# Optimization experiments

Hardware: AMD Instinct MI355X
Metric: run time of the kernel (lower is better)

## Reference

```python
import jax, jax.numpy as jnp
import numpy as np

WIDTH = 64  # attention_width

def setup_inputs() -> dict:
    key = jax.random.key(0)
    ks = jax.random.split(key, 4)
    B, T, D, U = 4, 1024, 1024, 64
    x = jax.random.normal(ks[0], (B, T, D), dtype=jnp.float32)
    Wt = jax.random.normal(ks[1], (D, U), dtype=jnp.float32) * (1.0 / np.sqrt(D))
    Wx = jax.random.normal(ks[2], (D, U), dtype=jnp.float32) * (1.0 / np.sqrt(D))
    bh = jnp.zeros((U,), dtype=jnp.float32)
    Wa = jax.random.normal(ks[3], (U, 1), dtype=jnp.float32) * (1.0 / np.sqrt(U))
    ba = jnp.zeros((1,), dtype=jnp.float32)
    return {"x": x, "Wt": Wt, "Wx": Wx, "bh": bh, "Wa": Wa, "ba": ba}


def reference(x, Wt, Wx, bh, Wa, ba):
    B, T, D = x.shape
    # additive emission: h = tanh(q_i + k_j + bh), e_ij = h @ Wa + ba
    q = jnp.einsum('btd,du->btu', x, Wt)  # [B,T,U]
    k = jnp.einsum('btd,du->btu', x, Wx)  # [B,T,U]
    h = jnp.tanh(q[:, :, None, :] + k[:, None, :, :] + bh)  # [B,T,T,U]
    e = jnp.einsum('btsu,uo->bts', h, Wa) + ba[0]  # [B,T,T]
    # local-width band mask (width centered, history_only=False)
    idx = jnp.arange(T)
    lower = (idx - WIDTH // 2)[:, None]           # [T,1]
    upper = lower + WIDTH
    band = (lower <= idx[None, :]) & (idx[None, :] < upper)  # [T,T]
    e = e - 10000.0 * (1.0 - band.astype(e.dtype))
    a = jax.nn.softmax(e, axis=-1)  # [B,T,T]
    v = jnp.einsum('bts,bsd->btd', a, x)
    return v
```

## Files before the change

### kernel.cpp

```cpp
#include <hip/hip_runtime.h>

#define BB 4
#define TT 1024
#define DD 1024
#define UU 64
#define HW 32

typedef unsigned short u16;
typedef __attribute__((ext_vector_type(4))) unsigned short u16x4;
typedef __attribute__((ext_vector_type(8))) unsigned short u16x8;
typedef __attribute__((ext_vector_type(8))) short bf16x8;
typedef __attribute__((ext_vector_type(4))) float f32x4;

__device__ __forceinline__ u16 bf16_rne(float f) {
  unsigned b = __builtin_bit_cast(unsigned, f);
  b += 0x7FFFu + ((b >> 16) & 1u);
  return (u16)(b >> 16);
}
__device__ __forceinline__ float bf16_tof(u16 h) {
  return __builtin_bit_cast(float, ((unsigned)h) << 16);
}

#define WLD 65
__global__ __launch_bounds__(256) void wprep_kernel(
    const float* __restrict__ Wt, const float* __restrict__ Wx,
    u16* __restrict__ Wht, u16* __restrict__ Wlt)
{
  __shared__ float ws[128 * WLD];
  const int tid = threadIdx.x;
  const int d0  = blockIdx.x * 128;
  const float* __restrict__ src = blockIdx.y ? Wx : Wt;

  for (int i = tid; i < 2048; i += 256) {
    int r  = i >> 4;
    int c4 = (i & 15) << 2;
    float4 v = *(const float4*)(src + (size_t)(d0 + r) * UU + c4);
    float* w = ws + r * WLD + c4;
    w[0] = v.x; w[1] = v.y; w[2] = v.z; w[3] = v.w;
  }
  __syncthreads();

  for (int it = tid; it < 1024; it += 256) {
    int u = it >> 4, oct = it & 15;
    u16x8 h, l;
    #pragma unroll
    for (int j = 0; j < 8; ++j) {
      float v = ws[(8 * oct + j) * WLD + u];
      u16 hh = bf16_rne(v);
      h[j] = hh;
      l[j] = bf16_rne(v - bf16_tof(hh));
    }
    size_t off = (size_t)(blockIdx.y * UU + u) * DD + d0 + 8 * oct;
    *(u16x8*)(Wht + off) = h;
    *(u16x8*)(Wlt + off) = l;
  }
}

#define PROWS 16
#define XLD (DD + 8)

__global__ __launch_bounds__(512) void proj_mfma_kernel(
    const float* __restrict__ x, const u16* __restrict__ Wht,
    const u16* __restrict__ Wlt, float* __restrict__ qo, float* __restrict__ ko)
{
  __shared__ __align__(16) u16 Xh[PROWS][XLD];
  __shared__ __align__(16) u16 Xl[PROWS][XLD];

  const int tid  = threadIdx.x;
  const int row0 = blockIdx.x * PROWS;

  {
    const float4* src = (const float4*)(x + (size_t)row0 * DD);
    #pragma unroll
    for (int i = 0; i < 8; ++i) {
      int idx4 = tid + 512 * i;
      int r    = idx4 >> 8;
      int k4   = (idx4 & 255) << 2;
      float4 v = src[idx4];
      float vv[4] = {v.x, v.y, v.z, v.w};
      u16x4 hv, lv;
      #pragma unroll
      for (int j = 0; j < 4; ++j) {
        u16 hh = bf16_rne(vv[j]);
        float lf = vv[j] - bf16_tof(hh);
        hv[j] = hh;
        lv[j] = bf16_rne(lf);
      }
      *(u16x4*)&Xh[r][k4] = hv;
      *(u16x4*)&Xl[r][k4] = lv;
    }
  }
  __syncthreads();

  const int lane = tid & 63;
  const int wv   = tid >> 6;
  const int arow = lane & 15;
  const int g    = lane >> 4;
  const int u0   = wv * 16;

  const u16* ah_p = &Xh[arow][8 * g];
  const u16* al_p = &Xl[arow][8 * g];
  const u16* bh_p = Wht + (size_t)(u0 + arow) * DD + 8 * g;
  const u16* bl_p = Wlt + (size_t)(u0 + arow) * DD + 8 * g;

  f32x4 acc0 = {0.f, 0.f, 0.f, 0.f};
  f32x4 acc1 = {0.f, 0.f, 0.f, 0.f};
  f32x4 acc2 = {0.f, 0.f, 0.f, 0.f};
  f32x4 acc3 = {0.f, 0.f, 0.f, 0.f};

  #pragma unroll 8
  for (int ks = 0; ks < 32; ++ks) {
    bf16x8 ah = *(const bf16x8*)(ah_p + 32 * ks);
    bf16x8 al = *(const bf16x8*)(al_p + 32 * ks);
    bf16x8 bh = *(const bf16x8*)(bh_p + 32 * ks);
    bf16x8 bl = *(const bf16x8*)(bl_p + 32 * ks);
    acc0 = __builtin_amdgcn_mfma_f32_16x16x32_bf16(ah, bh, acc0, 0, 0, 0);
    acc1 = __builtin_amdgcn_mfma_f32_16x16x32_bf16(ah, bl, acc1, 0, 0, 0);
    acc2 = __builtin_amdgcn_mfma_f32_16x16x32_bf16(al, bh, acc2, 0, 0, 0);
    acc3 = __builtin_amdgcn_mfma_f32_16x16x32_bf16(al, bl, acc3, 0, 0, 0);
  }

  const int col = u0 + arow;
  float* dst = (col < UU) ? (qo + col) : (ko + (col - UU));
  #pragma unroll
  for (int r = 0; r < 4; ++r) {
    dst[(size_t)(row0 + 4 * g + r) * UU] = acc0[r] + acc1[r] + acc2[r] + acc3[r];
  }
}

__global__ __launch_bounds__(512) void band_kernel(
    const float* __restrict__ x,  const float* __restrict__ qi,
    const float* __restrict__ ki, const float* __restrict__ bh,
    const float* __restrict__ Wa, const float* __restrict__ ba,
    float* __restrict__ out)
{
  __shared__ __align__(16) float eq[8 * UU];
  __shared__ __align__(16) float ek[72 * UU];
  __shared__ __align__(16) float at[72 * 8];

  const int tid  = threadIdx.x;
  const int bid  = blockIdx.x;
  const int tile = (bid & 7) * 64 + (bid >> 3);
  const int b    = tile >> 7;
  const int i0   = (tile & 127) * 8;

  const int jlo = max(0, i0 - HW);
  const int jhi = min(TT, i0 + 8 - 1 + HW);
  const int NJ  = jhi - jlo;

  {
    if (tid < 128) {
      float4 qv = ((const float4*)(qi + (size_t)(b * TT + i0) * UU))[tid];
      float4 bv = ((const float4*)bh)[tid & 15];
      float4 ev;
      ev.x = __expf(-2.0f * (qv.x + bv.x));
      ev.y = __expf(-2.0f * (qv.y + bv.y));
      ev.z = __expf(-2.0f * (qv.z + bv.z));
      ev.w = __expf(-2.0f * (qv.w + bv.w));
      ((float4*)eq)[tid] = ev;
    }
    const float4* ksrc = (const float4*)(ki + (size_t)(b * TT + jlo) * UU);
    const int nk4 = NJ * (UU / 4);
    for (int i2 = tid; i2 < nk4; i2 += 512) {
      float4 kv = ksrc[i2];
      float4 ev;
      ev.x = __expf(-2.0f * kv.x);
      ev.y = __expf(-2.0f * kv.y);
      ev.z = __expf(-2.0f * kv.z);
      ev.w = __expf(-2.0f * kv.w);
      ((float4*)ek)[i2] = ev;
    }
  }
  __syncthreads();

  const float bav = ba[0];

  {
    const int w    = tid >> 6;
    const int lane = tid & 63;
    const int g    = lane >> 3;
    const int uc   = (lane & 7) * 8;
    float eqv[8], wv[8];
    {
      float4 a0 = *(const float4*)(eq + g * UU + uc);
      float4 a1 = *(const float4*)(eq + g * UU + uc + 4);
      eqv[0] = a0.x; eqv[1] = a0.y; eqv[2] = a0.z; eqv[3] = a0.w;
      eqv[4] = a1.x; eqv[5] = a1.y; eqv[6] = a1.z; eqv[7] = a1.w;
      float4 wa0 = *(const float4*)(Wa + uc);
      float4 wa1 = *(const float4*)(Wa + uc + 4);
      wv[0] = wa0.x; wv[1] = wa0.y; wv[2] = wa0.z; wv[3] = wa0.w;
      wv[4] = wa1.x; wv[5] = wa1.y; wv[6] = wa1.z; wv[7] = wa1.w;
    }
    const int ig = i0 + g;
    for (int j = w; j < NJ; j += 8) {
      const float* kp = ek + j * UU + uc;
      float4 k0 = *(const float4*)kp;
      float4 k1 = *(const float4*)(kp + 4);
      float ekv[8] = {k0.x, k0.y, k0.z, k0.w, k1.x, k1.y, k1.z, k1.w};
      float s0 = 0.f;
      #pragma unroll
      for (int s = 0; s < 8; ++s) {
        float t  = eqv[s] * ekv[s];
        float th = (1.0f - t) * __builtin_amdgcn_rcpf(1.0f + t);
        s0 = __builtin_fmaf(th, wv[s], s0);
      }
      s0 += __shfl_xor(s0, 1);
      s0 += __shfl_xor(s0, 2);
      s0 += __shfl_xor(s0, 4);
      const int jg = jlo + j;
      const bool inband = (jg >= ig - HW) && (jg < ig + HW);
      if ((lane & 7) == 0) at[j * 8 + g] = inband ? (s0 + bav) : -1e30f;
    }
  }
  __syncthreads();

  {
    const int row = tid >> 6;
    const int l   = tid & 63;
    float v0 = (l      < NJ) ? at[(l     ) * 8 + row] : -1e30f;
    float v1 = (l + 64 < NJ) ? at[(l + 64) * 8 + row] : -1e30f;
    float m = fmaxf(v0, v1);
    #pragma unroll
    for (int off = 32; off >= 1; off >>= 1) m = fmaxf(m, __shfl_xor(m, off));
    float e0 = __expf(v0 - m);
    float e1 = __expf(v1 - m);
    float ssum = e0 + e1;
    #pragma unroll
    for (int off = 32; off >= 1; off >>= 1) ssum += __shfl_xor(ssum, off);
    float inv = 1.0f / ssum;
    if (l      < NJ) at[(l     ) * 8 + row] = e0 * inv;
    if (l + 64 < NJ) at[(l + 64) * 8 + row] = e1 * inv;
  }
  __syncthreads();

  {
    float2 vacc[8];
    #pragma unroll
    for (int i = 0; i < 8; ++i) vacc[i] = make_float2(0.f, 0.f);
    const float* xb = x + (size_t)(b * TT + jlo) * DD + 2 * tid;
    #pragma unroll 2
    for (int j = 0; j < NJ; ++j) {
      float2 xv = *(const float2*)(xb + (size_t)j * DD);
      float4 a0 = *(const float4*)(at + j * 8);
      float4 a1 = *(const float4*)(at + j * 8 + 4);
      float av[8] = {a0.x, a0.y, a0.z, a0.w, a1.x, a1.y, a1.z, a1.w};
      #pragma unroll
      for (int i = 0; i < 8; ++i) {
        vacc[i].x = __builtin_fmaf(av[i], xv.x, vacc[i].x);
        vacc[i].y = __builtin_fmaf(av[i], xv.y, vacc[i].y);
      }
    }
    float* ob = out + (size_t)(b * TT + i0) * DD + 2 * tid;
    #pragma unroll
    for (int i = 0; i < 8; ++i) *(float2*)(ob + (size_t)i * DD) = vacc[i];
  }
}

extern "C" void kernel_launch(void* const* d_in, const int* in_sizes, int n_in,
                              void* d_out, int out_size, void* d_ws, size_t ws_size,
                              hipStream_t stream) {
  const float* x  = (const float*)d_in[0];
  const float* Wt = (const float*)d_in[1];
  const float* Wx = (const float*)d_in[2];
  const float* bh = (const float*)d_in[3];
  const float* Wa = (const float*)d_in[4];
  const float* ba = (const float*)d_in[5];
  float* out = (float*)d_out;

  float* q = (float*)d_ws;
  float* k = q + (size_t)BB * TT * UU;
  u16* Wht = (u16*)(k + (size_t)BB * TT * UU);
  u16* Wlt = Wht + (size_t)128 * DD;

  wprep_kernel<<<dim3(8, 2), dim3(256), 0, stream>>>(Wt, Wx, Wht, Wlt);
  proj_mfma_kernel<<<dim3((BB * TT) / PROWS), dim3(512), 0, stream>>>(x, Wht, Wlt, q, k);
  band_kernel<<<dim3((BB * TT) / 8), dim3(512), 0, stream>>>(x, q, k, bh, Wa, ba, out);
}
```

Before: 117.1 us.

## Fuse bias and exp transform into projection epilogue, read eq/ek from global

Moves the exp(-2(q+bh)) and exp(-2k) transforms into the projection kernel's epilogue, so each value is computed once instead of recomputed by every overlapping band tile. The band kernel drops its shared-memory staging and one barrier, reading the transformed q/k directly from global (cache-resident). It also switches the value accumulation to a packed float2 vector form and raises the unroll from 2 to 4. The risk is uncoalesced per-lane global reads in the score loop, where shared memory was used before.

```diff
diff --git a/kernel.cpp b/kernel.cpp
--- a/kernel.cpp
+++ b/kernel.cpp
@@ -11,6 +11,7 @@
 typedef __attribute__((ext_vector_type(8))) unsigned short u16x8;
 typedef __attribute__((ext_vector_type(8))) short bf16x8;
 typedef __attribute__((ext_vector_type(4))) float f32x4;
+typedef __attribute__((ext_vector_type(2))) float f32x2;
 
 __device__ __forceinline__ u16 bf16_rne(float f) {
   unsigned b = __builtin_bit_cast(unsigned, f);
@@ -61,7 +62,8 @@
 
 __global__ __launch_bounds__(512) void proj_mfma_kernel(
     const float* __restrict__ x, const u16* __restrict__ Wht,
-    const u16* __restrict__ Wlt, float* __restrict__ qo, float* __restrict__ ko)
+    const u16* __restrict__ Wlt, const float* __restrict__ bh,
+    float* __restrict__ qo, float* __restrict__ ko)
 {
   __shared__ __align__(16) u16 Xh[PROWS][XLD];
   __shared__ __align__(16) u16 Xl[PROWS][XLD];
@@ -112,30 +114,29 @@
   for (int ks = 0; ks < 32; ++ks) {
     bf16x8 ah = *(const bf16x8*)(ah_p + 32 * ks);
     bf16x8 al = *(const bf16x8*)(al_p + 32 * ks);
-    bf16x8 bh = *(const bf16x8*)(bh_p + 32 * ks);
-    bf16x8 bl = *(const bf16x8*)(bl_p + 32 * ks);
-    acc0 = __builtin_amdgcn_mfma_f32_16x16x32_bf16(ah, bh, acc0, 0, 0, 0);
-    acc1 = __builtin_amdgcn_mfma_f32_16x16x32_bf16(ah, bl, acc1, 0, 0, 0);
-    acc2 = __builtin_amdgcn_mfma_f32_16x16x32_bf16(al, bh, acc2, 0, 0, 0);
-    acc3 = __builtin_amdgcn_mfma_f32_16x16x32_bf16(al, bl, acc3, 0, 0, 0);
-  }
-
-  const int col = u0 + arow;
+    bf16x8 bhv = *(const bf16x8*)(bh_p + 32 * ks);
+    bf16x8 blv = *(const bf16x8*)(bl_p + 32 * ks);
+    acc0 = __builtin_amdgcn_mfma_f32_16x16x32_bf16(ah, bhv, acc0, 0, 0, 0);
+    acc1 = __builtin_amdgcn_mfma_f32_16x16x32_bf16(ah, blv, acc1, 0, 0, 0);
+    acc2 = __builtin_amdgcn_mfma_f32_16x16x32_bf16(al, bhv, acc2, 0, 0, 0);
+    acc3 = __builtin_amdgcn_mfma_f32_16x16x32_bf16(al, blv, acc3, 0, 0, 0);
+  }
+
+  const int col  = u0 + arow;
+  const float bias = (col < UU) ? bh[col] : 0.0f;
   float* dst = (col < UU) ? (qo + col) : (ko + (col - UU));
   #pragma unroll
   for (int r = 0; r < 4; ++r) {
-    dst[(size_t)(row0 + 4 * g + r) * UU] = acc0[r] + acc1[r] + acc2[r] + acc3[r];
+    float v = acc0[r] + acc1[r] + acc2[r] + acc3[r];
+    dst[(size_t)(row0 + 4 * g + r) * UU] = __expf(-2.0f * (v + bias));
   }
 }
 
 __global__ __launch_bounds__(512) void band_kernel(
-    const float* __restrict__ x,  const float* __restrict__ qi,
-    const float* __restrict__ ki, const float* __restrict__ bh,
-    const float* __restrict__ Wa, const float* __restrict__ ba,
-    float* __restrict__ out)
+    const float* __restrict__ x,  const float* __restrict__ eqg,
+    const float* __restrict__ ekg, const float* __restrict__ Wa,
+    const float* __restrict__ ba, float* __restrict__ out)
 {
-  __shared__ __align__(16) float eq[8 * UU];
-  __shared__ __align__(16) float ek[72 * UU];
   __shared__ __align__(16) float at[72 * 8];
 
   const int tid  = threadIdx.x;
@@ -147,31 +148,6 @@
   const int jlo = max(0, i0 - HW);
   const int jhi = min(TT, i0 + 8 - 1 + HW);
   const int NJ  = jhi - jlo;
-
-  {
-    if (tid < 128) {
-      float4 qv = ((const float4*)(qi + (size_t)(b * TT + i0) * UU))[tid];
-      float4 bv = ((const float4*)bh)[tid & 15];
-      float4 ev;
-      ev.x = __expf(-2.0f * (qv.x + bv.x));
-      ev.y = __expf(-2.0f * (qv.y + bv.y));
-      ev.z = __expf(-2.0f * (qv.z + bv.z));
-      ev.w = __expf(-2.0f * (qv.w + bv.w));
-      ((float4*)eq)[tid] = ev;
-    }
-    const float4* ksrc = (const float4*)(ki + (size_t)(b * TT + jlo) * UU);
-    const int nk4 = NJ * (UU / 4);
-    for (int i2 = tid; i2 < nk4; i2 += 512) {
-      float4 kv = ksrc[i2];
-      float4 ev;
-      ev.x = __expf(-2.0f * kv.x);
-      ev.y = __expf(-2.0f * kv.y);
-      ev.z = __expf(-2.0f * kv.z);
-      ev.w = __expf(-2.0f * kv.w);
-      ((float4*)ek)[i2] = ev;
-    }
-  }
-  __syncthreads();
 
   const float bav = ba[0];
 
@@ -182,8 +158,9 @@
     const int uc   = (lane & 7) * 8;
     float eqv[8], wv[8];
     {
-      float4 a0 = *(const float4*)(eq + g * UU + uc);
-      float4 a1 = *(const float4*)(eq + g * UU + uc + 4);
+      const float* qp = eqg + (size_t)(b * TT + i0 + g) * UU + uc;
+      float4 a0 = *(const float4*)qp;
+      float4 a1 = *(const float4*)(qp + 4);
       eqv[0] = a0.x; eqv[1] = a0.y; eqv[2] = a0.z; eqv[3] = a0.w;
       eqv[4] = a1.x; eqv[5] = a1.y; eqv[6] = a1.z; eqv[7] = a1.w;
       float4 wa0 = *(const float4*)(Wa + uc);
@@ -192,8 +169,9 @@
       wv[4] = wa1.x; wv[5] = wa1.y; wv[6] = wa1.z; wv[7] = wa1.w;
     }
     const int ig = i0 + g;
+    const float* kbase = ekg + (size_t)(b * TT + jlo) * UU + uc;
     for (int j = w; j < NJ; j += 8) {
-      const float* kp = ek + j * UU + uc;
+      const float* kp = kbase + (size_t)j * UU;
       float4 k0 = *(const float4*)kp;
       float4 k1 = *(const float4*)(kp + 4);
       float ekv[8] = {k0.x, k0.y, k0.z, k0.w, k1.x, k1.y, k1.z, k1.w};
@@ -234,25 +212,26 @@
   __syncthreads();
 
   {
-    float2 vacc[8];
-    #pragma unroll
-    for (int i = 0; i < 8; ++i) vacc[i] = make_float2(0.f, 0.f);
+    const f32x2 z = {0.f, 0.f};
+    f32x2 vacc[8];
+    #pragma unroll
+    for (int i = 0; i < 8; ++i) vacc[i] = z;
     const float* xb = x + (size_t)(b * TT + jlo) * DD + 2 * tid;
-    #pragma unroll 2
+    #pragma unroll 4
     for (int j = 0; j < NJ; ++j) {
-      float2 xv = *(const float2*)(xb + (size_t)j * DD);
+      f32x2 xv = *(const f32x2*)(xb + (size_t)j * DD);
       float4 a0 = *(const float4*)(at + j * 8);
       float4 a1 = *(const float4*)(at + j * 8 + 4);
       float av[8] = {a0.x, a0.y, a0.z, a0.w, a1.x, a1.y, a1.z, a1.w};
       #pragma unroll
       for (int i = 0; i < 8; ++i) {
-        vacc[i].x = __builtin_fmaf(av[i], xv.x, vacc[i].x);
-        vacc[i].y = __builtin_fmaf(av[i], xv.y, vacc[i].y);
+        f32x2 s = {av[i], av[i]};
+        vacc[i] = s * xv + vacc[i];
       }
     }
     float* ob = out + (size_t)(b * TT + i0) * DD + 2 * tid;
     #pragma unroll
-    for (int i = 0; i < 8; ++i) *(float2*)(ob + (size_t)i * DD) = vacc[i];
+    for (int i = 0; i < 8; ++i) *(f32x2*)(ob + (size_t)i * DD) = vacc[i];
   }
 }
 
@@ -273,6 +252,6 @@
   u16* Wlt = Wht + (size_t)128 * DD;
 
   wprep_kernel<<<dim3(8, 2), dim3(256), 0, stream>>>(Wt, Wx, Wht, Wlt);
-  proj_mfma_kernel<<<dim3((BB * TT) / PROWS), dim3(512), 0, stream>>>(x, Wht, Wlt, q, k);
-  band_kernel<<<dim3((BB * TT) / 8), dim3(512), 0, stream>>>(x, q, k, bh, Wa, ba, out);
-}
+  proj_mfma_kernel<<<dim3((BB * TT) / PROWS), dim3(512), 0, stream>>>(x, Wht, Wlt, bh, q, k);
+  band_kernel<<<dim3((BB * TT) / 8), dim3(512), 0, stream>>>(x, q, k, Wa, ba, out);
+}
```

New measurement: 115.8 us (median of 2 runs). Within noise of the previous version (-1.1%).
